# Kernel optimization log

Measured on AMD Instinct MI355X. Metric: run time of the kernel, lower is better.

Reference implementation:

```python
import jax, jax.numpy as jnp
import numpy as np

N, V, H = 2048, 204, 160
LN_EPS = 1e-5


def setup_inputs() -> dict:
    key = jax.random.key(0)
    ks = jax.random.split(key, 5)
    x = jax.random.normal(ks[0], (N, V, 1), dtype=jnp.float32)
    fc1_w = jax.random.normal(ks[1], (V, H), dtype=jnp.float32) * 0.02
    fc1_b = jnp.zeros((V, H), dtype=jnp.float32)
    fc2_w = jax.random.normal(ks[2], (V, H, H), dtype=jnp.float32) * 0.02
    fc2_b = jnp.zeros((V, H), dtype=jnp.float32)
    glu_w = jax.random.normal(ks[3], (V, 2 * H, H), dtype=jnp.float32) * 0.02
    glu_b = jnp.zeros((V, 2 * H), dtype=jnp.float32)
    skip_w = jax.random.normal(ks[4], (V, H), dtype=jnp.float32) * 0.02
    skip_b = jnp.zeros((V, H), dtype=jnp.float32)
    ln_gamma = jnp.ones((H,), dtype=jnp.float32)
    ln_beta = jnp.zeros((H,), dtype=jnp.float32)
    return {"x": x, "fc1_w": fc1_w, "fc1_b": fc1_b, "fc2_w": fc2_w,
            "fc2_b": fc2_b, "glu_w": glu_w, "glu_b": glu_b,
            "skip_w": skip_w, "skip_b": skip_b,
            "ln_gamma": ln_gamma, "ln_beta": ln_beta}


def reference(x, fc1_w, fc1_b, fc2_w, fc2_b, glu_w, glu_b, skip_w, skip_b,
              ln_gamma, ln_beta):
    # x: (N, V, 1) -> xs: (N, V)
    xs = x[..., 0]
    # broadcast linear (var_dim=1 -> H): (N, V, H)
    h = jax.nn.elu(xs[:, :, None] * fc1_w[None] + fc1_b[None])
    # per-variable H x H GEMM: bmm over V
    h = jnp.einsum('nvh,vhk->nvk', h, fc2_w) + fc2_b[None]
    # GLU projection: (N, V, 2H)  (matches bmm(h, glu_w.transpose(1,2)))
    glu = jnp.einsum('nvh,vgh->nvg', h, glu_w) + glu_b[None]
    fc_out, gate = glu[..., :H], glu[..., H:]
    h = fc_out * jax.nn.sigmoid(gate)  # dropout is identity at eval
    # skip path (broadcast linear)
    skip = xs[:, :, None] * skip_w[None] + skip_b[None]
    y = skip + h
    # LayerNorm over last dim
    mu = jnp.mean(y, axis=-1, keepdims=True)
    var = jnp.mean(jnp.square(y - mu), axis=-1, keepdims=True)
    yhat = (y - mu) * jax.lax.rsqrt(var + LN_EPS)
    return yhat * ln_gamma + ln_beta
```

## Files before the change

kernel.cpp:

```cpp
#include <hip/hip_runtime.h>

#define N_TOK 2048
#define V_DIM 204
#define H_DIM 160
#define G_DIM 320
#define BM 128
#define LN_EPSF 1e-5f

typedef short s8v __attribute__((ext_vector_type(8)));
typedef unsigned short u16x8 __attribute__((ext_vector_type(8)));
typedef float f32x4 __attribute__((ext_vector_type(4)));

#define IMG_SUB 51200
#define IMG_PER_V (3 * IMG_SUB)

typedef unsigned int __attribute__((address_space(1))) as1_u32;
typedef unsigned int __attribute__((address_space(3))) as3_u32;

__device__ __forceinline__ void gl_lds16(const void* g, void* l) {
    __builtin_amdgcn_global_load_lds((as1_u32*)g, (as3_u32*)l, 16, 0, 0);
}

__device__ __forceinline__ unsigned short f2bf(float f) {
    union { float f; unsigned int u; } a;
    a.f = f;
    unsigned int r = a.u + 0x7fffu + ((a.u >> 16) & 1u);
    return (unsigned short)(r >> 16);
}

__global__ __launch_bounds__(256) void prep_weights(const float* __restrict__ fc2_w,
                                                    const float* __restrict__ glu_w,
                                                    unsigned short* __restrict__ ws) {
    int v = blockIdx.x;
    int t = threadIdx.x;
    __shared__ float tile[H_DIM][H_DIM + 1];
    const float* w1 = fc2_w + (size_t)v * H_DIM * H_DIM;
    for (int i = t; i < H_DIM * H_DIM; i += 256)
        tile[i / H_DIM][i % H_DIM] = w1[i];
    __syncthreads();
    char* img = (char*)ws + (size_t)v * IMG_PER_V;
    for (int c = t; c < 3200; c += 256) {
        int chunk = c / 160, kout = c % 160;
        u16x8 pk;
        #pragma unroll
        for (int j = 0; j < 8; j++) pk[j] = f2bf(tile[chunk * 8 + j][kout]);
        *(u16x8*)(img + (size_t)c * 16) = pk;
    }
    const float* w2 = glu_w + (size_t)v * G_DIM * H_DIM;
    for (int c = t; c < 6400; c += 256) {
        int chunk = c % 20, grow = (c / 20) % 160, half = c / 3200;
        const float* src = w2 + (size_t)(half * H_DIM + grow) * H_DIM + chunk * 8;
        f32x4 lo = *(const f32x4*)src;
        f32x4 hi = *(const f32x4*)(src + 4);
        u16x8 pk;
        #pragma unroll
        for (int j = 0; j < 4; j++) { pk[j] = f2bf(lo[j]); pk[4 + j] = f2bf(hi[j]); }
        *(u16x8*)(img + IMG_SUB + (size_t)half * IMG_SUB + (size_t)(chunk * 160 + grow) * 16) = pk;
    }
}

__global__ __launch_bounds__(512, 2) void grn_main(
    const float* __restrict__ x,
    const float* __restrict__ fc1_w, const float* __restrict__ fc1_b,
    const float* __restrict__ fc2_b, const float* __restrict__ glu_b,
    const float* __restrict__ skip_w, const float* __restrict__ skip_b,
    const float* __restrict__ ln_g, const float* __restrict__ ln_b,
    const unsigned short* __restrict__ ws, float* __restrict__ out)
{
    __shared__ __align__(16) unsigned short h_lds[20 * 128 * 8];
    __shared__ __align__(16) unsigned short w_lds[20 * 160 * 8];
    __shared__ __align__(16) unsigned short c1_lds[20 * 128 * 8];

    int bid = blockIdx.x;
    int swb = (bid & 7) * 408 + (bid >> 3);
    int v  = swb >> 4;
    int n0 = (swb & 15) * BM;

    int t = threadIdx.x;
    int lane = t & 63;
    int wv = t >> 6;
    int wr = wv >> 1;
    int wc = wv & 1;
    int col = lane & 15;
    int kg  = lane >> 4;

    const char* img = (const char*)ws + (size_t)v * IMG_PER_V;

    for (int i = t; i < 3200; i += 512)
        gl_lds16(img + (size_t)i * 16, (char*)w_lds + i * 16);

    const float* fw = fc1_w + v * H_DIM;
    const float* fb = fc1_b + v * H_DIM;
    for (int i = t; i < 2560; i += 512) {
        int chunk = i >> 7, row = i & 127;
        float xv = x[(size_t)(n0 + row) * V_DIM + v];
        int k0 = chunk * 8;
        u16x8 pk;
        #pragma unroll
        for (int j = 0; j < 8; j++) {
            float z = xv * fw[k0 + j] + fb[k0 + j];
            float e = z > 0.f ? z : (__expf(z) - 1.f);
            pk[j] = f2bf(e);
        }
        *(u16x8*)((char*)h_lds + chunk * 2048 + row * 16) = pk;
    }
    __syncthreads();

    s8v a1[2][5];
    #pragma unroll
    for (int m = 0; m < 2; m++)
        #pragma unroll
        for (int kk = 0; kk < 5; kk++)
            a1[m][kk] = *(const s8v*)((const char*)h_lds +
                         (kk * 4 + kg) * 2048 + (wr * 32 + m * 16 + col) * 16);

    f32x4 acc[2][5];
    #pragma unroll
    for (int m = 0; m < 2; m++)
        #pragma unroll
        for (int n = 0; n < 5; n++) acc[m][n] = (f32x4){0.f, 0.f, 0.f, 0.f};

    #pragma unroll
    for (int kk = 0; kk < 5; kk++) {
        s8v b[5];
        #pragma unroll
        for (int n = 0; n < 5; n++)
            b[n] = *(const s8v*)((const char*)w_lds +
                    (kk * 4 + kg) * 2560 + (wc * 80 + n * 16 + col) * 16);
        #pragma unroll
        for (int n = 0; n < 5; n++)
            #pragma unroll
            for (int m = 0; m < 2; m++)
                acc[m][n] = __builtin_amdgcn_mfma_f32_16x16x32_bf16(a1[m][kk], b[n], acc[m][n], 0, 0, 0);
    }
    __syncthreads();

    for (int i = t; i < 3200; i += 512)
        gl_lds16(img + IMG_SUB + (size_t)i * 16, (char*)w_lds + i * 16);

    const float* f2b = fc2_b + v * H_DIM;
    #pragma unroll
    for (int n = 0; n < 5; n++) {
        int gc = wc * 80 + n * 16 + col;
        float bias = f2b[gc];
        int cbase = (gc >> 3) * 2048 + (gc & 7) * 2;
        #pragma unroll
        for (int m = 0; m < 2; m++)
            #pragma unroll
            for (int j = 0; j < 4; j++) {
                int row = wr * 32 + m * 16 + kg * 4 + j;
                *(unsigned short*)((char*)c1_lds + cbase + row * 16) = f2bf(acc[m][n][j] + bias);
            }
    }
    __syncthreads();

    s8v a2[2][5];
    #pragma unroll
    for (int m = 0; m < 2; m++)
        #pragma unroll
        for (int kk = 0; kk < 5; kk++)
            a2[m][kk] = *(const s8v*)((const char*)c1_lds +
                         (kk * 4 + kg) * 2048 + (wr * 32 + m * 16 + col) * 16);

    f32x4 af[2][5];
    #pragma unroll
    for (int m = 0; m < 2; m++)
        #pragma unroll
        for (int n = 0; n < 5; n++) af[m][n] = (f32x4){0.f, 0.f, 0.f, 0.f};

    #pragma unroll
    for (int kk = 0; kk < 5; kk++) {
        s8v b[5];
        #pragma unroll
        for (int n = 0; n < 5; n++)
            b[n] = *(const s8v*)((const char*)w_lds +
                    (kk * 4 + kg) * 2560 + (wc * 80 + n * 16 + col) * 16);
        #pragma unroll
        for (int n = 0; n < 5; n++)
            #pragma unroll
            for (int m = 0; m < 2; m++)
                af[m][n] = __builtin_amdgcn_mfma_f32_16x16x32_bf16(a2[m][kk], b[n], af[m][n], 0, 0, 0);
    }
    __syncthreads();

    for (int i = t; i < 3200; i += 512)
        gl_lds16(img + 2 * IMG_SUB + (size_t)i * 16, (char*)w_lds + i * 16);
    __syncthreads();

    f32x4 ag[2][5];
    #pragma unroll
    for (int m = 0; m < 2; m++)
        #pragma unroll
        for (int n = 0; n < 5; n++) ag[m][n] = (f32x4){0.f, 0.f, 0.f, 0.f};

    #pragma unroll
    for (int kk = 0; kk < 5; kk++) {
        s8v b[5];
        #pragma unroll
        for (int n = 0; n < 5; n++)
            b[n] = *(const s8v*)((const char*)w_lds +
                    (kk * 4 + kg) * 2560 + (wc * 80 + n * 16 + col) * 16);
        #pragma unroll
        for (int n = 0; n < 5; n++)
            #pragma unroll
            for (int m = 0; m < 2; m++)
                ag[m][n] = __builtin_amdgcn_mfma_f32_16x16x32_bf16(a2[m][kk], b[n], ag[m][n], 0, 0, 0);
    }

    const float* gb  = glu_b + v * G_DIM;
    const float* sw_ = skip_w + v * H_DIM;
    const float* sb_ = skip_b + v * H_DIM;

    float xr[2][4];
    #pragma unroll
    for (int m = 0; m < 2; m++)
        #pragma unroll
        for (int j = 0; j < 4; j++)
            xr[m][j] = x[(size_t)(n0 + wr * 32 + m * 16 + kg * 4 + j) * V_DIM + v];

    float y[2][5][4];
    float sum[2][4] = {}, ssq[2][4] = {};
    #pragma unroll
    for (int n = 0; n < 5; n++) {
        int gc = wc * 80 + n * 16 + col;
        float bfo = gb[gc], bga = gb[H_DIM + gc];
        float sww = sw_[gc], sbb = sb_[gc];
        #pragma unroll
        for (int m = 0; m < 2; m++)
            #pragma unroll
            for (int j = 0; j < 4; j++) {
                float fo = af[m][n][j] + bfo;
                float ga = ag[m][n][j] + bga;
                float hh = fo / (1.f + __expf(-ga));
                float yv = xr[m][j] * sww + sbb + hh;
                y[m][n][j] = yv;
                sum[m][j] += yv;
                ssq[m][j] += yv * yv;
            }
    }
    #pragma unroll
    for (int msk = 1; msk < 16; msk <<= 1)
        #pragma unroll
        for (int m = 0; m < 2; m++)
            #pragma unroll
            for (int j = 0; j < 4; j++) {
                sum[m][j] += __shfl_xor(sum[m][j], msk, 64);
                ssq[m][j] += __shfl_xor(ssq[m][j], msk, 64);
            }

    float2* red = (float2*)h_lds;
    if (col == 0) {
        #pragma unroll
        for (int m = 0; m < 2; m++)
            #pragma unroll
            for (int j = 0; j < 4; j++) {
                int row = wr * 32 + m * 16 + kg * 4 + j;
                red[row * 2 + wc] = make_float2(sum[m][j], ssq[m][j]);
            }
    }
    __syncthreads();

    float mu_[2][4], rs_[2][4];
    #pragma unroll
    for (int m = 0; m < 2; m++)
        #pragma unroll
        for (int j = 0; j < 4; j++) {
            int row = wr * 32 + m * 16 + kg * 4 + j;
            f32x4 p = *(const f32x4*)&red[row * 2];
            float mu = (p[0] + p[2]) * (1.f / H_DIM);
            float var = (p[1] + p[3]) * (1.f / H_DIM) - mu * mu;
            mu_[m][j] = mu;
            rs_[m][j] = rsqrtf(var + LN_EPSF);
        }

    #pragma unroll
    for (int n = 0; n < 5; n++) {
        int gc = wc * 80 + n * 16 + col;
        float g = ln_g[gc], be = ln_b[gc];
        #pragma unroll
        for (int m = 0; m < 2; m++)
            #pragma unroll
            for (int j = 0; j < 4; j++) {
                int row = n0 + wr * 32 + m * 16 + kg * 4 + j;
                float val = (y[m][n][j] - mu_[m][j]) * rs_[m][j] * g + be;
                __builtin_nontemporal_store(val, &out[((size_t)row * V_DIM + v) * H_DIM + gc]);
            }
    }
}

__global__ __launch_bounds__(160) void grn_fallback(
    const float* __restrict__ x,
    const float* __restrict__ fc1_w, const float* __restrict__ fc1_b,
    const float* __restrict__ fc2_w, const float* __restrict__ fc2_b,
    const float* __restrict__ glu_w, const float* __restrict__ glu_b,
    const float* __restrict__ skip_w, const float* __restrict__ skip_b,
    const float* __restrict__ ln_g, const float* __restrict__ ln_b,
    float* __restrict__ out)
{
    int n = blockIdx.x / V_DIM, v = blockIdx.x % V_DIM;
    int k = threadIdx.x;
    __shared__ float hb[H_DIM], c1[H_DIM], yb[H_DIM];
    float xv = x[(size_t)n * V_DIM + v];
    float z = xv * fc1_w[v * H_DIM + k] + fc1_b[v * H_DIM + k];
    hb[k] = z > 0.f ? z : (__expf(z) - 1.f);
    __syncthreads();
    const float* w1 = fc2_w + (size_t)v * H_DIM * H_DIM;
    float s = fc2_b[v * H_DIM + k];
    for (int i = 0; i < H_DIM; i++) s += hb[i] * w1[(size_t)i * H_DIM + k];
    c1[k] = s;
    __syncthreads();
    const float* w2 = glu_w + (size_t)v * G_DIM * H_DIM;
    float sf = glu_b[v * G_DIM + k], sg = glu_b[v * G_DIM + H_DIM + k];
    for (int i = 0; i < H_DIM; i++) {
        float cv = c1[i];
        sf += cv * w2[(size_t)k * H_DIM + i];
        sg += cv * w2[(size_t)(k + H_DIM) * H_DIM + i];
    }
    float y = xv * skip_w[v * H_DIM + k] + skip_b[v * H_DIM + k] + sf / (1.f + __expf(-sg));
    yb[k] = y;
    __syncthreads();
    float sum = 0.f, ssq = 0.f;
    for (int i = 0; i < H_DIM; i++) { sum += yb[i]; ssq += yb[i] * yb[i]; }
    float mu = sum / H_DIM;
    float var = ssq / H_DIM - mu * mu;
    out[((size_t)n * V_DIM + v) * H_DIM + k] =
        (y - mu) * rsqrtf(var + LN_EPSF) * ln_g[k] + ln_b[k];
}

extern "C" void kernel_launch(void* const* d_in, const int* in_sizes, int n_in,
                              void* d_out, int out_size, void* d_ws, size_t ws_size,
                              hipStream_t stream) {
    const float* x      = (const float*)d_in[0];
    const float* fc1_w  = (const float*)d_in[1];
    const float* fc1_b  = (const float*)d_in[2];
    const float* fc2_w  = (const float*)d_in[3];
    const float* fc2_b  = (const float*)d_in[4];
    const float* glu_w  = (const float*)d_in[5];
    const float* glu_b  = (const float*)d_in[6];
    const float* skip_w = (const float*)d_in[7];
    const float* skip_b = (const float*)d_in[8];
    const float* ln_g   = (const float*)d_in[9];
    const float* ln_b   = (const float*)d_in[10];
    float* out = (float*)d_out;

    size_t need = (size_t)V_DIM * IMG_PER_V;
    if (ws_size >= need) {
        unsigned short* ws = (unsigned short*)d_ws;
        prep_weights<<<V_DIM, 256, 0, stream>>>(fc2_w, glu_w, ws);
        grn_main<<<V_DIM * (N_TOK / BM), 512, 0, stream>>>(
            x, fc1_w, fc1_b, fc2_b, glu_b, skip_w, skip_b, ln_g, ln_b, ws, out);
    } else {
        grn_fallback<<<N_TOK * V_DIM, 160, 0, stream>>>(
            x, fc1_w, fc1_b, fc2_w, fc2_b, glu_w, glu_b, skip_w, skip_b, ln_g, ln_b, out);
    }
}
```

Baseline: 556.8 us.

## Halve token tile, merge activation buffers, split weight prep into quarter-blocks

```diff
diff --git a/kernel.cpp b/kernel.cpp
--- a/kernel.cpp
+++ b/kernel.cpp
@@ -4,7 +4,7 @@
 #define V_DIM 204
 #define H_DIM 160
 #define G_DIM 320
-#define BM 128
+#define BM 64
 #define LN_EPSF 1e-5f
 
 typedef short s8v __attribute__((ext_vector_type(8)));
@@ -31,35 +31,43 @@
 __global__ __launch_bounds__(256) void prep_weights(const float* __restrict__ fc2_w,
                                                     const float* __restrict__ glu_w,
                                                     unsigned short* __restrict__ ws) {
-    int v = blockIdx.x;
+    int b = blockIdx.x;
+    int v = b >> 2, p = b & 3;
     int t = threadIdx.x;
-    __shared__ float tile[H_DIM][H_DIM + 1];
-    const float* w1 = fc2_w + (size_t)v * H_DIM * H_DIM;
-    for (int i = t; i < H_DIM * H_DIM; i += 256)
-        tile[i / H_DIM][i % H_DIM] = w1[i];
-    __syncthreads();
     char* img = (char*)ws + (size_t)v * IMG_PER_V;
-    for (int c = t; c < 3200; c += 256) {
-        int chunk = c / 160, kout = c % 160;
-        u16x8 pk;
-        #pragma unroll
-        for (int j = 0; j < 8; j++) pk[j] = f2bf(tile[chunk * 8 + j][kout]);
-        *(u16x8*)(img + (size_t)c * 16) = pk;
-    }
-    const float* w2 = glu_w + (size_t)v * G_DIM * H_DIM;
-    for (int c = t; c < 6400; c += 256) {
-        int chunk = c % 20, grow = (c / 20) % 160, half = c / 3200;
-        const float* src = w2 + (size_t)(half * H_DIM + grow) * H_DIM + chunk * 8;
-        f32x4 lo = *(const f32x4*)src;
-        f32x4 hi = *(const f32x4*)(src + 4);
-        u16x8 pk;
-        #pragma unroll
-        for (int j = 0; j < 4; j++) { pk[j] = f2bf(lo[j]); pk[4 + j] = f2bf(hi[j]); }
-        *(u16x8*)(img + IMG_SUB + (size_t)half * IMG_SUB + (size_t)(chunk * 160 + grow) * 16) = pk;
-    }
-}
-
-__global__ __launch_bounds__(512, 2) void grn_main(
+    if (p < 2) {
+        __shared__ float tile[H_DIM][81];
+        const float* w1 = fc2_w + (size_t)v * H_DIM * H_DIM + p * 80;
+        for (int i = t; i < H_DIM * 80; i += 256) {
+            int r = i / 80, c = i % 80;
+            tile[r][c] = w1[(size_t)r * H_DIM + c];
+        }
+        __syncthreads();
+        for (int c2 = t; c2 < 20 * 80; c2 += 256) {
+            int chunk = c2 / 80, ko = c2 % 80;
+            u16x8 pk;
+            #pragma unroll
+            for (int j = 0; j < 8; j++) pk[j] = f2bf(tile[chunk * 8 + j][ko]);
+            *(u16x8*)(img + (size_t)(chunk * 160 + p * 80 + ko) * 16) = pk;
+        }
+    } else {
+        int half = p - 2;
+        const float* w2 = glu_w + (size_t)v * G_DIM * H_DIM + (size_t)half * H_DIM * H_DIM;
+        char* dst = img + IMG_SUB + (size_t)half * IMG_SUB;
+        for (int c = t; c < 3200; c += 256) {
+            int grow = c / 20, chunk = c % 20;
+            const float* src = w2 + (size_t)grow * H_DIM + chunk * 8;
+            f32x4 lo = *(const f32x4*)src;
+            f32x4 hi = *(const f32x4*)(src + 4);
+            u16x8 pk;
+            #pragma unroll
+            for (int j = 0; j < 4; j++) { pk[j] = f2bf(lo[j]); pk[4 + j] = f2bf(hi[j]); }
+            *(u16x8*)(dst + (size_t)(chunk * 160 + grow) * 16) = pk;
+        }
+    }
+}
+
+__global__ __launch_bounds__(256, 2) void grn_main(
     const float* __restrict__ x,
     const float* __restrict__ fc1_w, const float* __restrict__ fc1_b,
     const float* __restrict__ fc2_b, const float* __restrict__ glu_b,
@@ -67,14 +75,13 @@
     const float* __restrict__ ln_g, const float* __restrict__ ln_b,
     const unsigned short* __restrict__ ws, float* __restrict__ out)
 {
-    __shared__ __align__(16) unsigned short h_lds[20 * 128 * 8];
     __shared__ __align__(16) unsigned short w_lds[20 * 160 * 8];
-    __shared__ __align__(16) unsigned short c1_lds[20 * 128 * 8];
+    __shared__ __align__(16) unsigned short hc_lds[20 * 64 * 8];
 
     int bid = blockIdx.x;
-    int swb = (bid & 7) * 408 + (bid >> 3);
-    int v  = swb >> 4;
-    int n0 = (swb & 15) * BM;
+    int swb = (bid & 7) * 816 + (bid >> 3);
+    int v  = swb >> 5;
+    int n0 = (swb & 31) * BM;
 
     int t = threadIdx.x;
     int lane = t & 63;
@@ -86,13 +93,13 @@
 
     const char* img = (const char*)ws + (size_t)v * IMG_PER_V;
 
-    for (int i = t; i < 3200; i += 512)
+    for (int i = t; i < 3200; i += 256)
         gl_lds16(img + (size_t)i * 16, (char*)w_lds + i * 16);
 
     const float* fw = fc1_w + v * H_DIM;
     const float* fb = fc1_b + v * H_DIM;
-    for (int i = t; i < 2560; i += 512) {
-        int chunk = i >> 7, row = i & 127;
+    for (int i = t; i < 20 * BM; i += 256) {
+        int chunk = i >> 6, row = i & 63;
         float xv = x[(size_t)(n0 + row) * V_DIM + v];
         int k0 = chunk * 8;
         u16x8 pk;
@@ -102,17 +109,19 @@
             float e = z > 0.f ? z : (__expf(z) - 1.f);
             pk[j] = f2bf(e);
         }
-        *(u16x8*)((char*)h_lds + chunk * 2048 + row * 16) = pk;
-    }
-    __syncthreads();
+        *(u16x8*)((char*)hc_lds + chunk * 1024 + row * 16) = pk;
+    }
+    __syncthreads();
+
+    int arow = wr * 32 + col;
 
     s8v a1[2][5];
     #pragma unroll
     for (int m = 0; m < 2; m++)
         #pragma unroll
         for (int kk = 0; kk < 5; kk++)
-            a1[m][kk] = *(const s8v*)((const char*)h_lds +
-                         (kk * 4 + kg) * 2048 + (wr * 32 + m * 16 + col) * 16);
+            a1[m][kk] = *(const s8v*)((const char*)hc_lds +
+                         (kk * 4 + kg) * 1024 + (arow + m * 16) * 16);
 
     f32x4 acc[2][5];
     #pragma unroll
@@ -135,7 +144,7 @@
     }
     __syncthreads();
 
-    for (int i = t; i < 3200; i += 512)
+    for (int i = t; i < 3200; i += 256)
         gl_lds16(img + IMG_SUB + (size_t)i * 16, (char*)w_lds + i * 16);
 
     const float* f2b = fc2_b + v * H_DIM;
@@ -143,13 +152,13 @@
     for (int n = 0; n < 5; n++) {
         int gc = wc * 80 + n * 16 + col;
         float bias = f2b[gc];
-        int cbase = (gc >> 3) * 2048 + (gc & 7) * 2;
+        int cbase = (gc >> 3) * 1024 + (gc & 7) * 2;
         #pragma unroll
         for (int m = 0; m < 2; m++)
             #pragma unroll
             for (int j = 0; j < 4; j++) {
                 int row = wr * 32 + m * 16 + kg * 4 + j;
-                *(unsigned short*)((char*)c1_lds + cbase + row * 16) = f2bf(acc[m][n][j] + bias);
+                *(unsigned short*)((char*)hc_lds + cbase + row * 16) = f2bf(acc[m][n][j] + bias);
             }
     }
     __syncthreads();
@@ -159,8 +168,8 @@
     for (int m = 0; m < 2; m++)
         #pragma unroll
         for (int kk = 0; kk < 5; kk++)
-            a2[m][kk] = *(const s8v*)((const char*)c1_lds +
-                         (kk * 4 + kg) * 2048 + (wr * 32 + m * 16 + col) * 16);
+            a2[m][kk] = *(const s8v*)((const char*)hc_lds +
+                         (kk * 4 + kg) * 1024 + (arow + m * 16) * 16);
 
     f32x4 af[2][5];
     #pragma unroll
@@ -183,56 +192,60 @@
     }
     __syncthreads();
 
-    for (int i = t; i < 3200; i += 512)
+    for (int i = t; i < 3200; i += 256)
         gl_lds16(img + 2 * IMG_SUB + (size_t)i * 16, (char*)w_lds + i * 16);
-    __syncthreads();
-
-    f32x4 ag[2][5];
-    #pragma unroll
-    for (int m = 0; m < 2; m++)
-        #pragma unroll
-        for (int n = 0; n < 5; n++) ag[m][n] = (f32x4){0.f, 0.f, 0.f, 0.f};
-
-    #pragma unroll
-    for (int kk = 0; kk < 5; kk++) {
-        s8v b[5];
-        #pragma unroll
-        for (int n = 0; n < 5; n++)
-            b[n] = *(const s8v*)((const char*)w_lds +
-                    (kk * 4 + kg) * 2560 + (wc * 80 + n * 16 + col) * 16);
-        #pragma unroll
-        for (int n = 0; n < 5; n++)
-            #pragma unroll
-            for (int m = 0; m < 2; m++)
-                ag[m][n] = __builtin_amdgcn_mfma_f32_16x16x32_bf16(a2[m][kk], b[n], ag[m][n], 0, 0, 0);
-    }
 
     const float* gb  = glu_b + v * G_DIM;
     const float* sw_ = skip_w + v * H_DIM;
     const float* sb_ = skip_b + v * H_DIM;
-
-    float xr[2][4];
+    float bfo[5], bga[5], sww[5], sbb[5], lng[5], lnb[5];
+    #pragma unroll
+    for (int n = 0; n < 5; n++) {
+        int gc = wc * 80 + n * 16 + col;
+        bfo[n] = gb[gc]; bga[n] = gb[H_DIM + gc];
+        sww[n] = sw_[gc]; sbb[n] = sb_[gc];
+        lng[n] = ln_g[gc]; lnb[n] = ln_b[gc];
+    }
+    float xrow[2][4];
     #pragma unroll
     for (int m = 0; m < 2; m++)
         #pragma unroll
         for (int j = 0; j < 4; j++)
-            xr[m][j] = x[(size_t)(n0 + wr * 32 + m * 16 + kg * 4 + j) * V_DIM + v];
+            xrow[m][j] = x[(size_t)(n0 + wr * 32 + m * 16 + kg * 4 + j) * V_DIM + v];
+    __syncthreads();
+
+    f32x4 ag[2][5];
+    #pragma unroll
+    for (int m = 0; m < 2; m++)
+        #pragma unroll
+        for (int n = 0; n < 5; n++) ag[m][n] = (f32x4){0.f, 0.f, 0.f, 0.f};
+
+    #pragma unroll
+    for (int kk = 0; kk < 5; kk++) {
+        s8v b[5];
+        #pragma unroll
+        for (int n = 0; n < 5; n++)
+            b[n] = *(const s8v*)((const char*)w_lds +
+                    (kk * 4 + kg) * 2560 + (wc * 80 + n * 16 + col) * 16);
+        #pragma unroll
+        for (int n = 0; n < 5; n++)
+            #pragma unroll
+            for (int m = 0; m < 2; m++)
+                ag[m][n] = __builtin_amdgcn_mfma_f32_16x16x32_bf16(a2[m][kk], b[n], ag[m][n], 0, 0, 0);
+    }
 
     float y[2][5][4];
     float sum[2][4] = {}, ssq[2][4] = {};
     #pragma unroll
     for (int n = 0; n < 5; n++) {
-        int gc = wc * 80 + n * 16 + col;
-        float bfo = gb[gc], bga = gb[H_DIM + gc];
-        float sww = sw_[gc], sbb = sb_[gc];
-        #pragma unroll
-        for (int m = 0; m < 2; m++)
-            #pragma unroll
-            for (int j = 0; j < 4; j++) {
-                float fo = af[m][n][j] + bfo;
-                float ga = ag[m][n][j] + bga;
+        #pragma unroll
+        for (int m = 0; m < 2; m++)
+            #pragma unroll
+            for (int j = 0; j < 4; j++) {
+                float fo = af[m][n][j] + bfo[n];
+                float ga = ag[m][n][j] + bga[n];
                 float hh = fo / (1.f + __expf(-ga));
-                float yv = xr[m][j] * sww + sbb + hh;
+                float yv = xrow[m][j] * sww[n] + sbb[n] + hh;
                 y[m][n][j] = yv;
                 sum[m][j] += yv;
                 ssq[m][j] += yv * yv;
@@ -248,7 +261,7 @@
                 ssq[m][j] += __shfl_xor(ssq[m][j], msk, 64);
             }
 
-    float2* red = (float2*)h_lds;
+    float2* red = (float2*)hc_lds;
     if (col == 0) {
         #pragma unroll
         for (int m = 0; m < 2; m++)
@@ -276,14 +289,13 @@
     #pragma unroll
     for (int n = 0; n < 5; n++) {
         int gc = wc * 80 + n * 16 + col;
-        float g = ln_g[gc], be = ln_b[gc];
         #pragma unroll
         for (int m = 0; m < 2; m++)
             #pragma unroll
             for (int j = 0; j < 4; j++) {
                 int row = n0 + wr * 32 + m * 16 + kg * 4 + j;
-                float val = (y[m][n][j] - mu_[m][j]) * rs_[m][j] * g + be;
-                __builtin_nontemporal_store(val, &out[((size_t)row * V_DIM + v) * H_DIM + gc]);
+                out[((size_t)row * V_DIM + v) * H_DIM + gc] =
+                    (y[m][n][j] - mu_[m][j]) * rs_[m][j] * lng[n] + lnb[n];
             }
     }
 }
@@ -346,8 +358,8 @@
     size_t need = (size_t)V_DIM * IMG_PER_V;
     if (ws_size >= need) {
         unsigned short* ws = (unsigned short*)d_ws;
-        prep_weights<<<V_DIM, 256, 0, stream>>>(fc2_w, glu_w, ws);
-        grn_main<<<V_DIM * (N_TOK / BM), 512, 0, stream>>>(
+        prep_weights<<<V_DIM * 4, 256, 0, stream>>>(fc2_w, glu_w, ws);
+        grn_main<<<V_DIM * (N_TOK / BM), 256, 0, stream>>>(
             x, fc1_w, fc1_b, fc2_b, glu_b, skip_w, skip_b, ln_g, ln_b, ws, out);
     } else {
         grn_fallback<<<N_TOK * V_DIM, 160, 0, stream>>>(
```

New measurement: 541.9 us. -2.7%, faster.
